# Performance work log

Hardware: AMD Instinct MI355X
Metric: run time of the kernel (lower is better)

## Reference

```python
import jax, jax.numpy as jnp
import numpy as np

B, S, D, H, V, F, L = 16, 512, 768, 8, 100, 2048, 6
DH = D // H


def setup_inputs() -> dict:
    key = jax.random.key(0)
    ks = jax.random.split(key, 16)
    g = lambda k, shape: jax.random.normal(k, shape, jnp.float32) * 0.02
    return {
        "latent": jax.random.normal(ks[0], (B, D), jnp.float32),
        "target": jax.random.randint(ks[1], (B, S), 0, V),
        "tok_emb": g(ks[2], (V, D)),
        "pos_emb": g(ks[3], (S, D)),
        "sa_w_qkv": g(ks[4], (L, 3 * D, D)), "sa_b_qkv": jnp.zeros((L, 3 * D)),
        "sa_w_o": g(ks[5], (L, D, D)), "sa_b_o": jnp.zeros((L, D)),
        "ca_w_qkv": g(ks[6], (L, 3 * D, D)), "ca_b_qkv": jnp.zeros((L, 3 * D)),
        "ca_w_o": g(ks[7], (L, D, D)), "ca_b_o": jnp.zeros((L, D)),
        "ffn_w1": g(ks[8], (L, F, D)), "ffn_b1": jnp.zeros((L, F)),
        "ffn_w2": g(ks[9], (L, D, F)), "ffn_b2": jnp.zeros((L, D)),
        "ln1_g": jnp.ones((L, D)), "ln1_b": jnp.zeros((L, D)),
        "ln2_g": jnp.ones((L, D)), "ln2_b": jnp.zeros((L, D)),
        "ln3_g": jnp.ones((L, D)), "ln3_b": jnp.zeros((L, D)),
        "out_w": g(ks[10], (V, D)), "out_b": jnp.zeros((V,)),
    }


def _ln(x, g, b, eps=1e-5):
    mu = jnp.mean(x, axis=-1, keepdims=True)
    var = jnp.var(x, axis=-1, keepdims=True)
    return (x - mu) * jax.lax.rsqrt(var + eps) * g + b


def _mha(x_q, x_kv, w_qkv, b_qkv, w_o, b_o, causal):
    # torch MHA packed in_proj: rows [q; k; v]
    wq, wk, wv = jnp.split(w_qkv, 3, axis=0)
    bq, bk, bv = jnp.split(b_qkv, 3)
    Sq, Sk = x_q.shape[1], x_kv.shape[1]
    q = (x_q @ wq.T + bq).reshape(B, Sq, H, DH).transpose(0, 2, 1, 3)
    k = (x_kv @ wk.T + bk).reshape(B, Sk, H, DH).transpose(0, 2, 1, 3)
    v = (x_kv @ wv.T + bv).reshape(B, Sk, H, DH).transpose(0, 2, 1, 3)
    scores = jnp.einsum("bhqd,bhkd->bhqk", q, k) / jnp.sqrt(jnp.asarray(DH, q.dtype))
    if causal:
        mask = jnp.tril(jnp.ones((Sq, Sk), bool))
        scores = jnp.where(mask, scores, jnp.asarray(-1e9, scores.dtype))
    attn = jax.nn.softmax(scores, axis=-1)
    out = jnp.einsum("bhqk,bhkd->bhqd", attn, v).transpose(0, 2, 1, 3).reshape(B, Sq, D)
    return out @ w_o.T + b_o


def reference(latent, target, tok_emb, pos_emb,
              sa_w_qkv, sa_b_qkv, sa_w_o, sa_b_o,
              ca_w_qkv, ca_b_qkv, ca_w_o, ca_b_o,
              ffn_w1, ffn_b1, ffn_w2, ffn_b2,
              ln1_g, ln1_b, ln2_g, ln2_b, ln3_g, ln3_b,
              out_w, out_b):
    # decoder input: token + position embeddings
    x = tok_emb[target] + pos_emb[None, :S, :]  # [B,S,D]
    # memory = latent expanded along seq (as in torch forward)
    mem = jnp.broadcast_to(latent[:, None, :], (B, S, D))
    for i in range(L):  # post-norm TransformerDecoderLayer, dropout=0 (eval)
        x = _ln(x + _mha(x, x, sa_w_qkv[i], sa_b_qkv[i], sa_w_o[i], sa_b_o[i], True), ln1_g[i], ln1_b[i])
        x = _ln(x + _mha(x, mem, ca_w_qkv[i], ca_b_qkv[i], ca_w_o[i], ca_b_o[i], False), ln2_g[i], ln2_b[i])
        h = jax.nn.relu(x @ ffn_w1[i].T + ffn_b1[i]) @ ffn_w2[i].T + ffn_b2[i]
        x = _ln(x + h, ln3_g[i], ln3_b[i])
    return x @ out_w.T + out_b  # [B,S,V] logits
```

## Files before the change

kernel.cpp:

```cpp
#include <hip/hip_runtime.h>
#include <hip/hip_bf16.h>

#define BB 16
#define SS 512
#define DD 768
#define HH 8
#define VV 100
#define FF 2048
#define LL 6
#define DHH 96
#define TT (BB * SS)
#define BH (BB * HH)

typedef __bf16 bf16x8 __attribute__((ext_vector_type(8)));
typedef float f32x4 __attribute__((ext_vector_type(4)));
typedef __hip_bfloat16 bf16_t;

__global__ void cvt_kernel(const float* __restrict__ s, bf16_t* __restrict__ d, int n) {
    int i = blockIdx.x * blockDim.x + threadIdx.x;
    int stride = gridDim.x * blockDim.x;
    for (; i < n; i += stride) d[i] = __float2bfloat16(s[i]);
}

__global__ void fill_zero_kernel(uint4* __restrict__ p, int n) {
    int i = blockIdx.x * blockDim.x + threadIdx.x;
    if (i < n) p[i] = uint4{0u, 0u, 0u, 0u};
}

__global__ void pad_wout_kernel(const float* __restrict__ s, bf16_t* __restrict__ d) {
    int i = blockIdx.x * blockDim.x + threadIdx.x;
    int row = i / DD;
    d[i] = (row < VV) ? __float2bfloat16(s[i]) : __float2bfloat16(0.f);
}

__global__ void embed_kernel(const int* __restrict__ target,
                             const float* __restrict__ tok_emb,
                             const float* __restrict__ pos_emb,
                             float* __restrict__ x, bf16_t* __restrict__ xb) {
    int t = blockIdx.x;
    int s = t & (SS - 1);
    int tok = target[t];
    const float* te = tok_emb + (size_t)tok * DD;
    const float* pe = pos_emb + (size_t)s * DD;
    for (int d = threadIdx.x; d < DD; d += blockDim.x) {
        float v = te[d] + pe[d];
        x[(size_t)t * DD + d] = v;
        xb[(size_t)t * DD + d] = __float2bfloat16(v);
    }
}

__global__ void cv_kernel(const float* __restrict__ latent,
                          const float* __restrict__ ca_w_qkv,
                          const float* __restrict__ ca_b_qkv,
                          const float* __restrict__ ca_w_o,
                          const float* __restrict__ ca_b_o,
                          float* __restrict__ cv) {
    int i = blockIdx.x >> 4;
    int b = blockIdx.x & 15;
    __shared__ float lat[DD];
    __shared__ float vv[DD];
    const float* wv = ca_w_qkv + (size_t)i * 3 * DD * DD + (size_t)2 * DD * DD;
    const float* bv = ca_b_qkv + (size_t)i * 3 * DD + 2 * DD;
    const float* wo = ca_w_o + (size_t)i * DD * DD;
    const float* bo = ca_b_o + (size_t)i * DD;
    int tid = threadIdx.x;
    for (int d = tid; d < DD; d += blockDim.x) lat[d] = latent[(size_t)b * DD + d];
    __syncthreads();
    for (int j = tid; j < DD; j += blockDim.x) {
        const float4* wr = reinterpret_cast<const float4*>(wv + (size_t)j * DD);
        const float4* lp = reinterpret_cast<const float4*>(lat);
        float a = 0.f;
        for (int d = 0; d < DD / 4; ++d) {
            float4 w4 = wr[d], l4 = lp[d];
            a += w4.x * l4.x + w4.y * l4.y + w4.z * l4.z + w4.w * l4.w;
        }
        vv[j] = a + bv[j];
    }
    __syncthreads();
    for (int j = tid; j < DD; j += blockDim.x) {
        const float4* wr = reinterpret_cast<const float4*>(wo + (size_t)j * DD);
        const float4* vp = reinterpret_cast<const float4*>(vv);
        float a = 0.f;
        for (int d = 0; d < DD / 4; ++d) {
            float4 w4 = wr[d], v4 = vp[d];
            a += w4.x * v4.x + w4.y * v4.y + w4.z * v4.z + w4.w * v4.w;
        }
        cv[((size_t)i * BB + b) * DD + j] = a + bo[j];
    }
}

template <bool RELU, bool BOUT, bool RES>
__global__ __launch_bounds__(256, 3) void gemm_bt(
    const bf16_t* __restrict__ A, const bf16_t* __restrict__ W,
    const float* __restrict__ bias, const float* __restrict__ resid,
    float* __restrict__ Cf, bf16_t* __restrict__ Cb,
    int K, int ldc, int Nreal) {
    __shared__ uint4 As4[128 * 8];
    __shared__ uint4 Bs4[128 * 8];
    const int tid = threadIdx.x;
    const int m0 = blockIdx.y * 128;
    const int n0 = blockIdx.x * 128;
    const int lane = tid & 63, wave = tid >> 6;
    const int wr = wave >> 1, wc = wave & 1;
    const int r = lane & 15, q = lane >> 4;

    f32x4 acc[4][4];
#pragma unroll
    for (int i = 0; i < 4; ++i)
#pragma unroll
        for (int j = 0; j < 4; ++j) acc[i][j] = f32x4{0.f, 0.f, 0.f, 0.f};

    for (int k0 = 0; k0 < K; k0 += 64) {
#pragma unroll
        for (int it = 0; it < 4; ++it) {
            int c = tid + it * 256;
            int row = c >> 3, kc = c & 7;
            uint4 va = *reinterpret_cast<const uint4*>(A + (size_t)(m0 + row) * K + k0 + kc * 8);
            uint4 vb = *reinterpret_cast<const uint4*>(W + (size_t)(n0 + row) * K + k0 + kc * 8);
            int pc = kc ^ (row & 7);
            As4[row * 8 + pc] = va;
            Bs4[row * 8 + pc] = vb;
        }
        __syncthreads();
#pragma unroll
        for (int kk = 0; kk < 2; ++kk) {
            bf16x8 af[4], bfr[4];
            int lc = kk * 4 + q;
#pragma unroll
            for (int i = 0; i < 4; ++i) {
                int rowA = wr * 64 + i * 16 + r;
                af[i] = *reinterpret_cast<const bf16x8*>(&As4[rowA * 8 + (lc ^ (rowA & 7))]);
                int rowB = wc * 64 + i * 16 + r;
                bfr[i] = *reinterpret_cast<const bf16x8*>(&Bs4[rowB * 8 + (lc ^ (rowB & 7))]);
            }
#pragma unroll
            for (int i = 0; i < 4; ++i)
#pragma unroll
                for (int j = 0; j < 4; ++j)
                    acc[i][j] = __builtin_amdgcn_mfma_f32_16x16x32_bf16(af[i], bfr[j], acc[i][j], 0, 0, 0);
        }
        __syncthreads();
    }

#pragma unroll
    for (int i = 0; i < 4; ++i) {
#pragma unroll
        for (int j = 0; j < 4; ++j) {
            int cc = n0 + wc * 64 + j * 16 + r;
            if (cc < Nreal) {
                float bv = bias[cc];
#pragma unroll
                for (int reg = 0; reg < 4; ++reg) {
                    int rr = m0 + wr * 64 + i * 16 + q * 4 + reg;
                    float v = acc[i][j][reg] + bv;
                    if (RES) v += resid[(size_t)rr * ldc + cc];
                    if (RELU) v = fmaxf(v, 0.f);
                    if (BOUT) Cb[(size_t)rr * ldc + cc] = __float2bfloat16(v);
                    else Cf[(size_t)rr * ldc + cc] = v;
                }
            }
        }
    }
}

__global__ __launch_bounds__(256, 3) void gemm_qkv(
    const bf16_t* __restrict__ A, const bf16_t* __restrict__ W,
    const float* __restrict__ bias,
    bf16_t* __restrict__ Qh, bf16_t* __restrict__ Kh, bf16_t* __restrict__ Vt) {
    __shared__ uint4 As4[128 * 8];
    __shared__ uint4 Bs4[128 * 8];
    const int tid = threadIdx.x;
    const int m0 = blockIdx.y * 128;
    const int n0 = blockIdx.x * 128;
    const int lane = tid & 63, wave = tid >> 6;
    const int wr = wave >> 1, wc = wave & 1;
    const int r = lane & 15, q = lane >> 4;
    const int K = DD;

    f32x4 acc[4][4];
#pragma unroll
    for (int i = 0; i < 4; ++i)
#pragma unroll
        for (int j = 0; j < 4; ++j) acc[i][j] = f32x4{0.f, 0.f, 0.f, 0.f};

    for (int k0 = 0; k0 < K; k0 += 64) {
#pragma unroll
        for (int it = 0; it < 4; ++it) {
            int c = tid + it * 256;
            int row = c >> 3, kc = c & 7;
            uint4 va = *reinterpret_cast<const uint4*>(A + (size_t)(m0 + row) * K + k0 + kc * 8);
            uint4 vb = *reinterpret_cast<const uint4*>(W + (size_t)(n0 + row) * K + k0 + kc * 8);
            int pc = kc ^ (row & 7);
            As4[row * 8 + pc] = va;
            Bs4[row * 8 + pc] = vb;
        }
        __syncthreads();
#pragma unroll
        for (int kk = 0; kk < 2; ++kk) {
            bf16x8 af[4], bfr[4];
            int lc = kk * 4 + q;
#pragma unroll
            for (int i = 0; i < 4; ++i) {
                int rowA = wr * 64 + i * 16 + r;
                af[i] = *reinterpret_cast<const bf16x8*>(&As4[rowA * 8 + (lc ^ (rowA & 7))]);
                int rowB = wc * 64 + i * 16 + r;
                bfr[i] = *reinterpret_cast<const bf16x8*>(&Bs4[rowB * 8 + (lc ^ (rowB & 7))]);
            }
#pragma unroll
            for (int i = 0; i < 4; ++i)
#pragma unroll
                for (int j = 0; j < 4; ++j)
                    acc[i][j] = __builtin_amdgcn_mfma_f32_16x16x32_bf16(af[i], bfr[j], acc[i][j], 0, 0, 0);
        }
        __syncthreads();
    }

    const float scale = 0.10206207261596575f;
#pragma unroll
    for (int i = 0; i < 4; ++i) {
#pragma unroll
        for (int j = 0; j < 4; ++j) {
            int cc = n0 + wc * 64 + j * 16 + r;
            float bv = bias[cc];
            int sec = cc / DD;
            int within = cc - sec * DD;
            int hh = within / DHH;
            int dd = within - hh * DHH;
#pragma unroll
            for (int reg = 0; reg < 4; ++reg) {
                int rr = m0 + wr * 64 + i * 16 + q * 4 + reg;
                float v = acc[i][j][reg] + bv;
                int b = rr >> 9, s = rr & 511;
                int bh = b * HH + hh;
                if (sec == 0)
                    Qh[((size_t)bh * SS + s) * 128 + dd] = __float2bfloat16(v * scale);
                else if (sec == 1)
                    Kh[((size_t)bh * SS + s) * 128 + dd] = __float2bfloat16(v);
                else
                    Vt[((size_t)bh * 128 + dd) * SS + s] = __float2bfloat16(v);
            }
        }
    }
}

__global__ __launch_bounds__(256, 3) void gemm_sc(
    const bf16_t* __restrict__ Qh, const bf16_t* __restrict__ Kh,
    bf16_t* __restrict__ Scb) {
    const int bh = blockIdx.z;
    const int m0 = blockIdx.y * 128;
    const int n0 = blockIdx.x * 128;
    if (n0 > m0) return;
    const bf16_t* A = Qh + (size_t)bh * SS * 128;
    const bf16_t* W = Kh + (size_t)bh * SS * 128;
    __shared__ uint4 As4[128 * 8];
    __shared__ uint4 Bs4[128 * 8];
    const int tid = threadIdx.x;
    const int lane = tid & 63, wave = tid >> 6;
    const int wr = wave >> 1, wc = wave & 1;
    const int r = lane & 15, q = lane >> 4;
    const int K = 128;

    f32x4 acc[4][4];
#pragma unroll
    for (int i = 0; i < 4; ++i)
#pragma unroll
        for (int j = 0; j < 4; ++j) acc[i][j] = f32x4{0.f, 0.f, 0.f, 0.f};

    for (int k0 = 0; k0 < K; k0 += 64) {
#pragma unroll
        for (int it = 0; it < 4; ++it) {
            int c = tid + it * 256;
            int row = c >> 3, kc = c & 7;
            uint4 va = *reinterpret_cast<const uint4*>(A + (size_t)(m0 + row) * K + k0 + kc * 8);
            uint4 vb = *reinterpret_cast<const uint4*>(W + (size_t)(n0 + row) * K + k0 + kc * 8);
            int pc = kc ^ (row & 7);
            As4[row * 8 + pc] = va;
            Bs4[row * 8 + pc] = vb;
        }
        __syncthreads();
#pragma unroll
        for (int kk = 0; kk < 2; ++kk) {
            bf16x8 af[4], bfr[4];
            int lc = kk * 4 + q;
#pragma unroll
            for (int i = 0; i < 4; ++i) {
                int rowA = wr * 64 + i * 16 + r;
                af[i] = *reinterpret_cast<const bf16x8*>(&As4[rowA * 8 + (lc ^ (rowA & 7))]);
                int rowB = wc * 64 + i * 16 + r;
                bfr[i] = *reinterpret_cast<const bf16x8*>(&Bs4[rowB * 8 + (lc ^ (rowB & 7))]);
            }
#pragma unroll
            for (int i = 0; i < 4; ++i)
#pragma unroll
                for (int j = 0; j < 4; ++j)
                    acc[i][j] = __builtin_amdgcn_mfma_f32_16x16x32_bf16(af[i], bfr[j], acc[i][j], 0, 0, 0);
        }
        __syncthreads();
    }

    bf16_t* out = Scb + (size_t)bh * SS * SS;
#pragma unroll
    for (int i = 0; i < 4; ++i) {
#pragma unroll
        for (int j = 0; j < 4; ++j) {
            int cc = n0 + wc * 64 + j * 16 + r;
#pragma unroll
            for (int reg = 0; reg < 4; ++reg) {
                int rr = m0 + wr * 64 + i * 16 + q * 4 + reg;
                out[(size_t)rr * SS + cc] = __float2bfloat16(acc[i][j][reg]);
            }
        }
    }
}

__global__ __launch_bounds__(256) void softmax_kernel(bf16_t* __restrict__ Scb) {
    const int wave = threadIdx.x >> 6, lane = threadIdx.x & 63;
    const int row = blockIdx.x * 4 + wave;
    const int qpos = row & (SS - 1);
    const int kn = qpos + 1;
    bf16_t* rp = Scb + (size_t)row * SS;
    union {
        uint4 v;
        bf16_t h[8];
    } u;
    u.v = *reinterpret_cast<const uint4*>(rp + lane * 8);
    float vals[8];
    float m = -1e30f;
#pragma unroll
    for (int e = 0; e < 8; ++e) {
        int j = lane * 8 + e;
        vals[e] = (j < kn) ? __bfloat162float(u.h[e]) : -1e30f;
        m = fmaxf(m, vals[e]);
    }
#pragma unroll
    for (int s = 1; s < 64; s <<= 1) m = fmaxf(m, __shfl_xor(m, s));
    float sum = 0.f;
#pragma unroll
    for (int e = 0; e < 8; ++e) {
        vals[e] = __expf(vals[e] - m);
        sum += vals[e];
    }
#pragma unroll
    for (int s = 1; s < 64; s <<= 1) sum += __shfl_xor(sum, s);
    const float inv = 1.f / sum;
#pragma unroll
    for (int e = 0; e < 8; ++e) u.h[e] = __float2bfloat16(vals[e] * inv);
    *reinterpret_cast<uint4*>(rp + lane * 8) = u.v;
}

__global__ __launch_bounds__(256, 3) void gemm_pv(
    const bf16_t* __restrict__ P, const bf16_t* __restrict__ Vt,
    bf16_t* __restrict__ ao) {
    const int bh = blockIdx.z;
    const int m0 = blockIdx.y * 128;
    const bf16_t* A = P + (size_t)bh * SS * SS;
    const bf16_t* W = Vt + (size_t)bh * 128 * SS;
    __shared__ uint4 As4[128 * 8];
    __shared__ uint4 Bs4[128 * 8];
    const int tid = threadIdx.x;
    const int lane = tid & 63, wave = tid >> 6;
    const int wr = wave >> 1, wc = wave & 1;
    const int r = lane & 15, q = lane >> 4;
    const int K = SS;

    f32x4 acc[4][4];
#pragma unroll
    for (int i = 0; i < 4; ++i)
#pragma unroll
        for (int j = 0; j < 4; ++j) acc[i][j] = f32x4{0.f, 0.f, 0.f, 0.f};

    for (int k0 = 0; k0 < K; k0 += 64) {
#pragma unroll
        for (int it = 0; it < 4; ++it) {
            int c = tid + it * 256;
            int row = c >> 3, kc = c & 7;
            uint4 va = *reinterpret_cast<const uint4*>(A + (size_t)(m0 + row) * K + k0 + kc * 8);
            uint4 vb = *reinterpret_cast<const uint4*>(W + (size_t)row * K + k0 + kc * 8);
            int pc = kc ^ (row & 7);
            As4[row * 8 + pc] = va;
            Bs4[row * 8 + pc] = vb;
        }
        __syncthreads();
#pragma unroll
        for (int kk = 0; kk < 2; ++kk) {
            bf16x8 af[4], bfr[4];
            int lc = kk * 4 + q;
#pragma unroll
            for (int i = 0; i < 4; ++i) {
                int rowA = wr * 64 + i * 16 + r;
                af[i] = *reinterpret_cast<const bf16x8*>(&As4[rowA * 8 + (lc ^ (rowA & 7))]);
                int rowB = wc * 64 + i * 16 + r;
                bfr[i] = *reinterpret_cast<const bf16x8*>(&Bs4[rowB * 8 + (lc ^ (rowB & 7))]);
            }
#pragma unroll
            for (int i = 0; i < 4; ++i)
#pragma unroll
                for (int j = 0; j < 4; ++j)
                    acc[i][j] = __builtin_amdgcn_mfma_f32_16x16x32_bf16(af[i], bfr[j], acc[i][j], 0, 0, 0);
        }
        __syncthreads();
    }

    const int b = bh >> 3, hh = bh & 7;
#pragma unroll
    for (int i = 0; i < 4; ++i) {
#pragma unroll
        for (int j = 0; j < 4; ++j) {
            int cc = wc * 64 + j * 16 + r;
            if (cc < DHH) {
#pragma unroll
                for (int reg = 0; reg < 4; ++reg) {
                    int s = m0 + wr * 64 + i * 16 + q * 4 + reg;
                    size_t t = (size_t)b * SS + s;
                    ao[t * DD + hh * DHH + cc] = __float2bfloat16(acc[i][j][reg]);
                }
            }
        }
    }
}

__global__ __launch_bounds__(256) void ln_kernel(const float* __restrict__ in,
                                                 const float* __restrict__ bc,
                                                 const float* __restrict__ g,
                                                 const float* __restrict__ beta,
                                                 float* __restrict__ xo,
                                                 bf16_t* __restrict__ xb) {
    const int row = blockIdx.x;
    const int tid = threadIdx.x;
    const float* ip = in + (size_t)row * DD;
    const float* bp = bc ? bc + (size_t)(row >> 9) * DD : nullptr;
    float v[3];
#pragma unroll
    for (int t = 0; t < 3; ++t) {
        int d = tid + t * 256;
        v[t] = ip[d] + (bp ? bp[d] : 0.f);
    }
    float s = v[0] + v[1] + v[2];
    float ss = v[0] * v[0] + v[1] * v[1] + v[2] * v[2];
    for (int off = 32; off > 0; off >>= 1) {
        s += __shfl_down(s, off);
        ss += __shfl_down(ss, off);
    }
    __shared__ float red[8];
    if ((tid & 63) == 0) {
        red[(tid >> 6) * 2] = s;
        red[(tid >> 6) * 2 + 1] = ss;
    }
    __syncthreads();
    s = red[0] + red[2] + red[4] + red[6];
    ss = red[1] + red[3] + red[5] + red[7];
    const float mean = s * (1.f / DD);
    const float var = ss * (1.f / DD) - mean * mean;
    const float rs = rsqrtf(var + 1e-5f);
#pragma unroll
    for (int t = 0; t < 3; ++t) {
        int d = tid + t * 256;
        float y = (v[t] - mean) * rs * g[d] + beta[d];
        xo[(size_t)row * DD + d] = y;
        xb[(size_t)row * DD + d] = __float2bfloat16(y);
    }
}

extern "C" void kernel_launch(void* const* d_in, const int* in_sizes, int n_in,
                              void* d_out, int out_size, void* d_ws, size_t ws_size,
                              hipStream_t stream) {
    (void)in_sizes; (void)n_in; (void)out_size; (void)ws_size;
    const float* latent   = (const float*)d_in[0];
    const int*   target   = (const int*)d_in[1];
    const float* tok_emb  = (const float*)d_in[2];
    const float* pos_emb  = (const float*)d_in[3];
    const float* sa_w_qkv = (const float*)d_in[4];
    const float* sa_b_qkv = (const float*)d_in[5];
    const float* sa_w_o   = (const float*)d_in[6];
    const float* sa_b_o   = (const float*)d_in[7];
    const float* ca_w_qkv = (const float*)d_in[8];
    const float* ca_b_qkv = (const float*)d_in[9];
    const float* ca_w_o   = (const float*)d_in[10];
    const float* ca_b_o   = (const float*)d_in[11];
    const float* ffn_w1   = (const float*)d_in[12];
    const float* ffn_b1   = (const float*)d_in[13];
    const float* ffn_w2   = (const float*)d_in[14];
    const float* ffn_b2   = (const float*)d_in[15];
    const float* ln1_g    = (const float*)d_in[16];
    const float* ln1_b    = (const float*)d_in[17];
    const float* ln2_g    = (const float*)d_in[18];
    const float* ln2_b    = (const float*)d_in[19];
    const float* ln3_g    = (const float*)d_in[20];
    const float* ln3_b    = (const float*)d_in[21];
    const float* out_w    = (const float*)d_in[22];
    const float* out_b    = (const float*)d_in[23];
    float* out = (float*)d_out;

    char* ws = (char*)d_ws;
    size_t off = 0;
    auto alloc = [&](size_t bytes) {
        void* p = ws + off;
        off += (bytes + 255) & ~(size_t)255;
        return p;
    };
    float*  x    = (float*)alloc((size_t)TT * DD * 4);
    bf16_t* xb   = (bf16_t*)alloc((size_t)TT * DD * 2);
    bf16_t* ao   = (bf16_t*)alloc((size_t)TT * DD * 2);
    float*  cv   = (float*)alloc((size_t)LL * BB * DD * 4);
    bf16_t* wqkv_b = (bf16_t*)alloc((size_t)LL * 3 * DD * DD * 2);
    bf16_t* wo_b   = (bf16_t*)alloc((size_t)LL * DD * DD * 2);
    bf16_t* w1_b   = (bf16_t*)alloc((size_t)LL * FF * DD * 2);
    bf16_t* w2_b   = (bf16_t*)alloc((size_t)LL * DD * FF * 2);
    bf16_t* wout_b = (bf16_t*)alloc((size_t)128 * DD * 2);
    char* attnR = (char*)alloc((size_t)BH * SS * 128 * 2 * 3 + (size_t)BH * SS * SS * 2);
    bf16_t* Qh  = (bf16_t*)attnR;
    bf16_t* Kh  = Qh + (size_t)BH * SS * 128;
    bf16_t* Vt  = Kh + (size_t)BH * SS * 128;
    bf16_t* Scb = Vt + (size_t)BH * 128 * SS;
    bf16_t* h   = Scb;
    float*  tmp = (float*)((char*)Scb + ((size_t)34 << 20));

    cvt_kernel<<<2048, 256, 0, stream>>>(sa_w_qkv, wqkv_b, LL * 3 * DD * DD);
    cvt_kernel<<<2048, 256, 0, stream>>>(sa_w_o, wo_b, LL * DD * DD);
    cvt_kernel<<<2048, 256, 0, stream>>>(ffn_w1, w1_b, LL * FF * DD);
    cvt_kernel<<<2048, 256, 0, stream>>>(ffn_w2, w2_b, LL * DD * FF);
    pad_wout_kernel<<<(128 * DD) / 256, 256, 0, stream>>>(out_w, wout_b);
    {
        int n4 = (int)(((size_t)BH * SS * 128 * 2 * 2) / 16);
        fill_zero_kernel<<<(n4 + 255) / 256, 256, 0, stream>>>((uint4*)Qh, n4);
    }

    cv_kernel<<<LL * BB, 256, 0, stream>>>(latent, ca_w_qkv, ca_b_qkv, ca_w_o, ca_b_o, cv);

    embed_kernel<<<TT, 256, 0, stream>>>(target, tok_emb, pos_emb, x, xb);

    for (int i = 0; i < LL; ++i) {
        gemm_qkv<<<dim3(3 * DD / 128, TT / 128), 256, 0, stream>>>(
            xb, wqkv_b + (size_t)i * 3 * DD * DD, sa_b_qkv + (size_t)i * 3 * DD,
            Qh, Kh, Vt);
        gemm_sc<<<dim3(4, 4, BH), 256, 0, stream>>>(Qh, Kh, Scb);
        softmax_kernel<<<(BH * SS) / 4, 256, 0, stream>>>(Scb);
        gemm_pv<<<dim3(1, 4, BH), 256, 0, stream>>>(Scb, Vt, ao);
        gemm_bt<false, false, true><<<dim3(DD / 128, TT / 128), 256, 0, stream>>>(
            ao, wo_b + (size_t)i * DD * DD, sa_b_o + (size_t)i * DD,
            x, tmp, nullptr, DD, DD, DD);
        ln_kernel<<<TT, 256, 0, stream>>>(tmp, nullptr, ln1_g + (size_t)i * DD,
                                          ln1_b + (size_t)i * DD, x, xb);
        ln_kernel<<<TT, 256, 0, stream>>>(x, cv + (size_t)i * BB * DD,
                                          ln2_g + (size_t)i * DD, ln2_b + (size_t)i * DD, x, xb);
        gemm_bt<true, true, false><<<dim3(FF / 128, TT / 128), 256, 0, stream>>>(
            xb, w1_b + (size_t)i * FF * DD, ffn_b1 + (size_t)i * FF,
            nullptr, nullptr, h, DD, FF, FF);
        gemm_bt<false, false, true><<<dim3(DD / 128, TT / 128), 256, 0, stream>>>(
            h, w2_b + (size_t)i * DD * FF, ffn_b2 + (size_t)i * DD,
            x, tmp, nullptr, FF, DD, DD);
        ln_kernel<<<TT, 256, 0, stream>>>(tmp, nullptr, ln3_g + (size_t)i * DD,
                                          ln3_b + (size_t)i * DD, x, xb);
    }

    gemm_bt<false, false, false><<<dim3(1, TT / 128), 256, 0, stream>>>(
        xb, wout_b, out_b, nullptr, out, nullptr, DD, VV, VV);
}
```

Baseline: 2.133 ms.

## Use direct global-to-LDS loads in GEMMs, fuse LN1+LN2, parallelize cross-attn precompute

All bf16 GEMM tile loaders now use global_load_lds to write 16-byte chunks straight into shared memory, keeping the XOR swizzle by permuting source addresses. This skips the trip through registers. The two back-to-back layernorms (LN1, then cross-attn add plus LN2) are fused into one kernel, removing a full read and write of the activation tensor per layer. The cross-attention constant vector is now computed by two wide matrix-vector kernels across many blocks instead of 96 serial blocks. The main risk is the correctness and alignment of the direct-LDS load path.

After: 1.920 ms. -10.0%, faster.

```diff
diff --git a/kernel.cpp b/kernel.cpp
--- a/kernel.cpp
+++ b/kernel.cpp
@@ -15,6 +15,12 @@
 typedef __bf16 bf16x8 __attribute__((ext_vector_type(8)));
 typedef float f32x4 __attribute__((ext_vector_type(4)));
 typedef __hip_bfloat16 bf16_t;
+
+__device__ __forceinline__ void load_lds16(const void* g, void* l) {
+    __builtin_amdgcn_global_load_lds(
+        (const __attribute__((address_space(1))) void*)g,
+        (__attribute__((address_space(3))) void*)l, 16, 0, 0);
+}
 
 __global__ void cvt_kernel(const float* __restrict__ s, bf16_t* __restrict__ d, int n) {
     int i = blockIdx.x * blockDim.x + threadIdx.x;
@@ -49,44 +55,34 @@
     }
 }
 
-__global__ void cv_kernel(const float* __restrict__ latent,
-                          const float* __restrict__ ca_w_qkv,
-                          const float* __restrict__ ca_b_qkv,
-                          const float* __restrict__ ca_w_o,
-                          const float* __restrict__ ca_b_o,
-                          float* __restrict__ cv) {
-    int i = blockIdx.x >> 4;
-    int b = blockIdx.x & 15;
-    __shared__ float lat[DD];
-    __shared__ float vv[DD];
-    const float* wv = ca_w_qkv + (size_t)i * 3 * DD * DD + (size_t)2 * DD * DD;
-    const float* bv = ca_b_qkv + (size_t)i * 3 * DD + 2 * DD;
-    const float* wo = ca_w_o + (size_t)i * DD * DD;
-    const float* bo = ca_b_o + (size_t)i * DD;
-    int tid = threadIdx.x;
-    for (int d = tid; d < DD; d += blockDim.x) lat[d] = latent[(size_t)b * DD + d];
+__global__ __launch_bounds__(256) void cvmm_kernel(
+    const float* __restrict__ in, int in_per_layer,
+    const float* __restrict__ Wbase, size_t w_stride, size_t w_off,
+    const float* __restrict__ bbase, size_t b_stride, size_t b_off,
+    float* __restrict__ outp) {
+    const int jc = blockIdx.x;
+    const int layer = blockIdx.y;
+    __shared__ float inb[BB][DD + 4];
+    const int tid = threadIdx.x;
+    const float* ip = in + (size_t)layer * in_per_layer;
+    for (int idx = tid; idx < BB * DD; idx += 256) {
+        int b = idx / DD, d = idx - b * DD;
+        inb[b][d] = ip[(size_t)b * DD + d];
+    }
     __syncthreads();
-    for (int j = tid; j < DD; j += blockDim.x) {
-        const float4* wr = reinterpret_cast<const float4*>(wv + (size_t)j * DD);
-        const float4* lp = reinterpret_cast<const float4*>(lat);
-        float a = 0.f;
-        for (int d = 0; d < DD / 4; ++d) {
-            float4 w4 = wr[d], l4 = lp[d];
-            a += w4.x * l4.x + w4.y * l4.y + w4.z * l4.z + w4.w * l4.w;
-        }
-        vv[j] = a + bv[j];
-    }
-    __syncthreads();
-    for (int j = tid; j < DD; j += blockDim.x) {
-        const float4* wr = reinterpret_cast<const float4*>(wo + (size_t)j * DD);
-        const float4* vp = reinterpret_cast<const float4*>(vv);
-        float a = 0.f;
-        for (int d = 0; d < DD / 4; ++d) {
-            float4 w4 = wr[d], v4 = vp[d];
-            a += w4.x * v4.x + w4.y * v4.y + w4.z * v4.z + w4.w * v4.w;
-        }
-        cv[((size_t)i * BB + b) * DD + j] = a + bo[j];
-    }
+    const int j = jc * 16 + (tid >> 4);
+    const int b = tid & 15;
+    const float4* w4 = reinterpret_cast<const float4*>(
+        Wbase + (size_t)layer * w_stride + w_off + (size_t)j * DD);
+    const float4* i4 = reinterpret_cast<const float4*>(&inb[b][0]);
+    float a = 0.f;
+#pragma unroll 4
+    for (int d = 0; d < DD / 4; ++d) {
+        float4 w = w4[d], xv = i4[d];
+        a += w.x * xv.x + w.y * xv.y + w.z * xv.z + w.w * xv.w;
+    }
+    a += bbase[(size_t)layer * b_stride + b_off + j];
+    outp[((size_t)layer * BB + b) * DD + j] = a;
 }
 
 template <bool RELU, bool BOUT, bool RES>
@@ -97,10 +93,9 @@
     int K, int ldc, int Nreal) {
     __shared__ uint4 As4[128 * 8];
     __shared__ uint4 Bs4[128 * 8];
-    const int tid = threadIdx.x;
     const int m0 = blockIdx.y * 128;
     const int n0 = blockIdx.x * 128;
-    const int lane = tid & 63, wave = tid >> 6;
+    const int lane = threadIdx.x & 63, wave = threadIdx.x >> 6;
     const int wr = wave >> 1, wc = wave & 1;
     const int r = lane & 15, q = lane >> 4;
 
@@ -113,13 +108,12 @@
     for (int k0 = 0; k0 < K; k0 += 64) {
 #pragma unroll
         for (int it = 0; it < 4; ++it) {
-            int c = tid + it * 256;
-            int row = c >> 3, kc = c & 7;
-            uint4 va = *reinterpret_cast<const uint4*>(A + (size_t)(m0 + row) * K + k0 + kc * 8);
-            uint4 vb = *reinterpret_cast<const uint4*>(W + (size_t)(n0 + row) * K + k0 + kc * 8);
-            int pc = kc ^ (row & 7);
-            As4[row * 8 + pc] = va;
-            Bs4[row * 8 + pc] = vb;
+            int base = it * 256 + wave * 64;
+            int c = base + lane;
+            int row = c >> 3, pc = c & 7;
+            int kc = pc ^ (row & 7);
+            load_lds16(A + (size_t)(m0 + row) * K + k0 + kc * 8, &As4[base]);
+            load_lds16(W + (size_t)(n0 + row) * K + k0 + kc * 8, &Bs4[base]);
         }
         __syncthreads();
 #pragma unroll
@@ -169,10 +163,9 @@
     bf16_t* __restrict__ Qh, bf16_t* __restrict__ Kh, bf16_t* __restrict__ Vt) {
     __shared__ uint4 As4[128 * 8];
     __shared__ uint4 Bs4[128 * 8];
-    const int tid = threadIdx.x;
     const int m0 = blockIdx.y * 128;
     const int n0 = blockIdx.x * 128;
-    const int lane = tid & 63, wave = tid >> 6;
+    const int lane = threadIdx.x & 63, wave = threadIdx.x >> 6;
     const int wr = wave >> 1, wc = wave & 1;
     const int r = lane & 15, q = lane >> 4;
     const int K = DD;
@@ -186,13 +179,12 @@
     for (int k0 = 0; k0 < K; k0 += 64) {
 #pragma unroll
         for (int it = 0; it < 4; ++it) {
-            int c = tid + it * 256;
-            int row = c >> 3, kc = c & 7;
-            uint4 va = *reinterpret_cast<const uint4*>(A + (size_t)(m0 + row) * K + k0 + kc * 8);
-            uint4 vb = *reinterpret_cast<const uint4*>(W + (size_t)(n0 + row) * K + k0 + kc * 8);
-            int pc = kc ^ (row & 7);
-            As4[row * 8 + pc] = va;
-            Bs4[row * 8 + pc] = vb;
+            int base = it * 256 + wave * 64;
+            int c = base + lane;
+            int row = c >> 3, pc = c & 7;
+            int kc = pc ^ (row & 7);
+            load_lds16(A + (size_t)(m0 + row) * K + k0 + kc * 8, &As4[base]);
+            load_lds16(W + (size_t)(n0 + row) * K + k0 + kc * 8, &Bs4[base]);
         }
         __syncthreads();
 #pragma unroll
@@ -254,8 +246,7 @@
     const bf16_t* W = Kh + (size_t)bh * SS * 128;
     __shared__ uint4 As4[128 * 8];
     __shared__ uint4 Bs4[128 * 8];
-    const int tid = threadIdx.x;
-    const int lane = tid & 63, wave = tid >> 6;
+    const int lane = threadIdx.x & 63, wave = threadIdx.x >> 6;
     const int wr = wave >> 1, wc = wave & 1;
     const int r = lane & 15, q = lane >> 4;
     const int K = 128;
@@ -269,13 +260,12 @@
     for (int k0 = 0; k0 < K; k0 += 64) {
 #pragma unroll
         for (int it = 0; it < 4; ++it) {
-            int c = tid + it * 256;
-            int row = c >> 3, kc = c & 7;
-            uint4 va = *reinterpret_cast<const uint4*>(A + (size_t)(m0 + row) * K + k0 + kc * 8);
-            uint4 vb = *reinterpret_cast<const uint4*>(W + (size_t)(n0 + row) * K + k0 + kc * 8);
-            int pc = kc ^ (row & 7);
-            As4[row * 8 + pc] = va;
-            Bs4[row * 8 + pc] = vb;
+            int base = it * 256 + wave * 64;
+            int c = base + lane;
+            int row = c >> 3, pc = c & 7;
+            int kc = pc ^ (row & 7);
+            load_lds16(A + (size_t)(m0 + row) * K + k0 + kc * 8, &As4[base]);
+            load_lds16(W + (size_t)(n0 + row) * K + k0 + kc * 8, &Bs4[base]);
         }
         __syncthreads();
 #pragma unroll
@@ -357,8 +347,7 @@
     const bf16_t* W = Vt + (size_t)bh * 128 * SS;
     __shared__ uint4 As4[128 * 8];
     __shared__ uint4 Bs4[128 * 8];
-    const int tid = threadIdx.x;
-    const int lane = tid & 63, wave = tid >> 6;
+    const int lane = threadIdx.x & 63, wave = threadIdx.x >> 6;
     const int wr = wave >> 1, wc = wave & 1;
     const int r = lane & 15, q = lane >> 4;
     const int K = SS;
@@ -372,13 +361,12 @@
     for (int k0 = 0; k0 < K; k0 += 64) {
 #pragma unroll
         for (int it = 0; it < 4; ++it) {
-            int c = tid + it * 256;
-            int row = c >> 3, kc = c & 7;
-            uint4 va = *reinterpret_cast<const uint4*>(A + (size_t)(m0 + row) * K + k0 + kc * 8);
-            uint4 vb = *reinterpret_cast<const uint4*>(W + (size_t)row * K + k0 + kc * 8);
-            int pc = kc ^ (row & 7);
-            As4[row * 8 + pc] = va;
-            Bs4[row * 8 + pc] = vb;
+            int base = it * 256 + wave * 64;
+            int c = base + lane;
+            int row = c >> 3, pc = c & 7;
+            int kc = pc ^ (row & 7);
+            load_lds16(A + (size_t)(m0 + row) * K + k0 + kc * 8, &As4[base]);
+            load_lds16(W + (size_t)row * K + k0 + kc * 8, &Bs4[base]);
         }
         __syncthreads();
 #pragma unroll
@@ -420,7 +408,6 @@
 }
 
 __global__ __launch_bounds__(256) void ln_kernel(const float* __restrict__ in,
-                                                 const float* __restrict__ bc,
                                                  const float* __restrict__ g,
                                                  const float* __restrict__ beta,
                                                  float* __restrict__ xo,
@@ -428,13 +415,9 @@
     const int row = blockIdx.x;
     const int tid = threadIdx.x;
     const float* ip = in + (size_t)row * DD;
-    const float* bp = bc ? bc + (size_t)(row >> 9) * DD : nullptr;
     float v[3];
 #pragma unroll
-    for (int t = 0; t < 3; ++t) {
-        int d = tid + t * 256;
-        v[t] = ip[d] + (bp ? bp[d] : 0.f);
-    }
+    for (int t = 0; t < 3; ++t) v[t] = ip[tid + t * 256];
     float s = v[0] + v[1] + v[2];
     float ss = v[0] * v[0] + v[1] * v[1] + v[2] * v[2];
     for (int off = 32; off > 0; off >>= 1) {
@@ -456,6 +439,69 @@
     for (int t = 0; t < 3; ++t) {
         int d = tid + t * 256;
         float y = (v[t] - mean) * rs * g[d] + beta[d];
+        xo[(size_t)row * DD + d] = y;
+        xb[(size_t)row * DD + d] = __float2bfloat16(y);
+    }
+}
+
+__global__ __launch_bounds__(256) void ln12_kernel(const float* __restrict__ in,
+                                                   const float* __restrict__ cvv,
+                                                   const float* __restrict__ g1,
+                                                   const float* __restrict__ b1,
+                                                   const float* __restrict__ g2,
+                                                   const float* __restrict__ b2,
+                                                   float* __restrict__ xo,
+                                                   bf16_t* __restrict__ xb) {
+    const int row = blockIdx.x;
+    const int tid = threadIdx.x;
+    const float* ip = in + (size_t)row * DD;
+    const float* cp = cvv + (size_t)(row >> 9) * DD;
+    __shared__ float red[8];
+    float v[3];
+#pragma unroll
+    for (int t = 0; t < 3; ++t) v[t] = ip[tid + t * 256];
+    float s = v[0] + v[1] + v[2];
+    float ss = v[0] * v[0] + v[1] * v[1] + v[2] * v[2];
+    for (int off = 32; off > 0; off >>= 1) {
+        s += __shfl_down(s, off);
+        ss += __shfl_down(ss, off);
+    }
+    if ((tid & 63) == 0) {
+        red[(tid >> 6) * 2] = s;
+        red[(tid >> 6) * 2 + 1] = ss;
+    }
+    __syncthreads();
+    s = red[0] + red[2] + red[4] + red[6];
+    ss = red[1] + red[3] + red[5] + red[7];
+    float mean = s * (1.f / DD);
+    float var = ss * (1.f / DD) - mean * mean;
+    float rs = rsqrtf(var + 1e-5f);
+#pragma unroll
+    for (int t = 0; t < 3; ++t) {
+        int d = tid + t * 256;
+        v[t] = (v[t] - mean) * rs * g1[d] + b1[d] + cp[d];
+    }
+    s = v[0] + v[1] + v[2];
+    ss = v[0] * v[0] + v[1] * v[1] + v[2] * v[2];
+    for (int off = 32; off > 0; off >>= 1) {
+        s += __shfl_down(s, off);
+        ss += __shfl_down(ss, off);
+    }
+    __syncthreads();
+    if ((tid & 63) == 0) {
+        red[(tid >> 6) * 2] = s;
+        red[(tid >> 6) * 2 + 1] = ss;
+    }
+    __syncthreads();
+    s = red[0] + red[2] + red[4] + red[6];
+    ss = red[1] + red[3] + red[5] + red[7];
+    mean = s * (1.f / DD);
+    var = ss * (1.f / DD) - mean * mean;
+    rs = rsqrtf(var + 1e-5f);
+#pragma unroll
+    for (int t = 0; t < 3; ++t) {
+        int d = tid + t * 256;
+        float y = (v[t] - mean) * rs * g2[d] + b2[d];
         xo[(size_t)row * DD + d] = y;
         xb[(size_t)row * DD + d] = __float2bfloat16(y);
     }
@@ -502,6 +548,7 @@
     bf16_t* xb   = (bf16_t*)alloc((size_t)TT * DD * 2);
     bf16_t* ao   = (bf16_t*)alloc((size_t)TT * DD * 2);
     float*  cv   = (float*)alloc((size_t)LL * BB * DD * 4);
+    float*  v16  = (float*)alloc((size_t)LL * BB * DD * 4);
     bf16_t* wqkv_b = (bf16_t*)alloc((size_t)LL * 3 * DD * DD * 2);
     bf16_t* wo_b   = (bf16_t*)alloc((size_t)LL * DD * DD * 2);
     bf16_t* w1_b   = (bf16_t*)alloc((size_t)LL * FF * DD * 2);
@@ -525,7 +572,12 @@
         fill_zero_kernel<<<(n4 + 255) / 256, 256, 0, stream>>>((uint4*)Qh, n4);
     }
 
-    cv_kernel<<<LL * BB, 256, 0, stream>>>(latent, ca_w_qkv, ca_b_qkv, ca_w_o, ca_b_o, cv);
+    cvmm_kernel<<<dim3(DD / 16, LL), 256, 0, stream>>>(
+        latent, 0, ca_w_qkv, (size_t)3 * DD * DD, (size_t)2 * DD * DD,
+        ca_b_qkv, (size_t)3 * DD, (size_t)2 * DD, v16);
+    cvmm_kernel<<<dim3(DD / 16, LL), 256, 0, stream>>>(
+        v16, BB * DD, ca_w_o, (size_t)DD * DD, 0,
+        ca_b_o, (size_t)DD, 0, cv);
 
     embed_kernel<<<TT, 256, 0, stream>>>(target, tok_emb, pos_emb, x, xb);
 
@@ -539,17 +591,17 @@
         gemm_bt<false, false, true><<<dim3(DD / 128, TT / 128), 256, 0, stream>>>(
             ao, wo_b + (size_t)i * DD * DD, sa_b_o + (size_t)i * DD,
             x, tmp, nullptr, DD, DD, DD);
-        ln_kernel<<<TT, 256, 0, stream>>>(tmp, nullptr, ln1_g + (size_t)i * DD,
-                                          ln1_b + (size_t)i * DD, x, xb);
-        ln_kernel<<<TT, 256, 0, stream>>>(x, cv + (size_t)i * BB * DD,
-                                          ln2_g + (size_t)i * DD, ln2_b + (size_t)i * DD, x, xb);
+        ln12_kernel<<<TT, 256, 0, stream>>>(tmp, cv + (size_t)i * BB * DD,
+                                            ln1_g + (size_t)i * DD, ln1_b + (size_t)i * DD,
+                                            ln2_g + (size_t)i * DD, ln2_b + (size_t)i * DD,
+                                            x, xb);
         gemm_bt<true, true, false><<<dim3(FF / 128, TT / 128), 256, 0, stream>>>(
             xb, w1_b + (size_t)i * FF * DD, ffn_b1 + (size_t)i * FF,
             nullptr, nullptr, h, DD, FF, FF);
         gemm_bt<false, false, true><<<dim3(DD / 128, TT / 128), 256, 0, stream>>>(
             h, w2_b + (size_t)i * DD * FF, ffn_b2 + (size_t)i * DD,
             x, tmp, nullptr, FF, DD, DD);
-        ln_kernel<<<TT, 256, 0, stream>>>(tmp, nullptr, ln3_g + (size_t)i * DD,
+        ln_kernel<<<TT, 256, 0, stream>>>(tmp, ln3_g + (size_t)i * DD,
                                           ln3_b + (size_t)i * DD, x, xb);
     }
 
```
